# Performance work log

Measured on AMD Instinct MI355X. Metric: run time of the kernel, lower is better.

The kernel has to match this reference:

```python
import jax, jax.numpy as jnp
import numpy as np

N, E, H, D = 50000, 200000, 4, 64  # nodes, directed input edges, heads, hidden_dim
NODE_IN, EDGE_IN = 6, 4


def _ln(x, g, b):
    m = x.mean(-1, keepdims=True)
    v = ((x - m) ** 2).mean(-1, keepdims=True)
    return (x - m) / jnp.sqrt(v + 1e-5) * g + b


def setup_inputs() -> dict:
    key = jax.random.key(0)
    ks = iter(jax.random.split(key, 48))
    def w(i, o):
        return jax.random.normal(next(ks), (i, o), jnp.float32) / np.sqrt(i)
    def b(o):
        return jnp.zeros((o,), jnp.float32)
    return {
        "x": jax.random.normal(next(ks), (N, NODE_IN), jnp.float32),
        "edge_attr": jax.random.normal(next(ks), (E, EDGE_IN), jnp.float32),
        "ne_w1": w(NODE_IN, D), "ne_b1": b(D), "ne_w2": w(D, D), "ne_b2": b(D),
        "ee_w1": w(EDGE_IN, D), "ee_b1": b(D), "ee_w2": w(D, D), "ee_b2": b(D),
        "lnc_g": jnp.ones((2 * D,), jnp.float32), "lnc_b": jnp.zeros((2 * D,), jnp.float32),
        "tq_w": w(2 * D, H * D), "tq_b": b(H * D),
        "tk_w": w(2 * D, H * D), "tk_b": b(H * D),
        "tv_w": w(2 * D, H * D), "tv_b": b(H * D),
        "ts_w": w(2 * D, H * D), "ts_b": b(H * D),
        "lnt_g": jnp.ones((H * D,), jnp.float32), "lnt_b": jnp.zeros((H * D,), jnp.float32),
        "pn_w": w(H * D, D), "pn_b": b(D),
        "pe_w": w(H * D, D), "pe_b": b(D),
        "ec_w1": w(2 * D, D), "ec_b1": b(D), "ec_w2": w(D, 1), "ec_b2": b(1),
        "edge_index": jax.random.randint(next(ks), (2, E), 0, N),
    }


def _forward(x, edge_index, edge_attr, ne_w1, ne_b1, ne_w2, ne_b2,
             ee_w1, ee_b1, ee_w2, ee_b2, lnc_g, lnc_b,
             tq_w, tq_b, tk_w, tk_b, tv_w, tv_b, ts_w, ts_b,
             lnt_g, lnt_b, pn_w, pn_b, pe_w, pe_b,
             ec_w1, ec_b1, ec_w2, ec_b2):
    # bidirectionalize edges
    send = jnp.concatenate([edge_index[0], edge_index[1]])   # [2E]
    recv = jnp.concatenate([edge_index[1], edge_index[0]])   # [2E]
    ea_bi = jnp.concatenate([edge_attr, edge_attr], axis=0)  # [2E, EDGE_IN]
    # 2-layer ReLU MLP encoders (make_mlp with default ReLU output activation)
    node = jax.nn.relu(jax.nn.relu(x @ ne_w1 + ne_b1) @ ne_w2 + ne_b2)        # [N, D]
    edge = jax.nn.relu(jax.nn.relu(ea_bi @ ee_w1 + ee_b1) @ ee_w2 + ee_b2)    # [2E, D]
    for _ in range(1):  # n_iterations = 1
        x0, e0 = node, edge
        agg = jax.ops.segment_sum(edge, recv, num_segments=N)                  # scatter_add
        comb = _ln(jnp.concatenate([node, agg - node], axis=1), lnc_g, lnc_b)  # [N, 2D]
        # TransformerConv(2D -> D, heads=H, concat=True, root_weight=True)
        q = (comb @ tq_w + tq_b).reshape(N, H, D)
        k = (comb @ tk_w + tk_b).reshape(N, H, D)
        v = (comb @ tv_w + tv_b).reshape(N, H, D)
        q_e = q[recv]; k_e = k[send]; v_e = v[send]                            # [2E, H, D]
        score = (q_e * k_e).sum(-1) / np.sqrt(D)                               # [2E, H]
        m = jax.lax.stop_gradient(jax.ops.segment_max(score, recv, num_segments=N))
        ex = jnp.exp(score - m[recv])
        denom = jax.ops.segment_sum(ex, recv, num_segments=N)
        alpha = ex / (denom[recv] + 1e-16)                                     # per-dst softmax
        attn = jax.ops.segment_sum(alpha[:, :, None] * v_e, recv, num_segments=N).reshape(N, H * D)
        outn = _ln(attn + comb @ ts_w + ts_b, lnt_g, lnt_b)                    # skip (root) + LN
        node = outn @ pn_w + pn_b + x0
        edge = (outn[send] - outn[recv]) @ pe_w + pe_b + e0
    start, end = edge_index[0], edge_index[1]
    clf = jnp.concatenate([node[start], node[end]], axis=1)                    # [E, 2D]
    return (jax.nn.relu(clf @ ec_w1 + ec_b1) @ ec_w2 + ec_b2).squeeze(-1)      # [E]


def reference(x, edge_attr, ne_w1, ne_b1, ne_w2, ne_b2, ee_w1, ee_b1, ee_w2, ee_b2,
              lnc_g, lnc_b, tq_w, tq_b, tk_w, tk_b, tv_w, tv_b, ts_w, ts_b,
              lnt_g, lnt_b, pn_w, pn_b, pe_w, pe_b, ec_w1, ec_b1, ec_w2, ec_b2,
              edge_index):
    return _forward(x, edge_index, edge_attr, ne_w1, ne_b1, ne_w2, ne_b2,
                    ee_w1, ee_b1, ee_w2, ee_b2, lnc_g, lnc_b,
                    tq_w, tq_b, tk_w, tk_b, tv_w, tv_b, ts_w, ts_b,
                    lnt_g, lnt_b, pn_w, pn_b, pe_w, pe_b,
                    ec_w1, ec_b1, ec_w2, ec_b2)
```

## Files before the change

### kernel.cpp

```cpp
#include <hip/hip_runtime.h>
#include <hip/hip_bf16.h>


typedef __attribute__((ext_vector_type(8))) short short8;
typedef __attribute__((ext_vector_type(8))) unsigned short u16x8;
typedef __attribute__((ext_vector_type(4))) float f32x4;

__device__ __forceinline__ float wave_reduce_sum(float p) {
  #pragma unroll
  for (int o = 32; o; o >>= 1) p += __shfl_xor(p, o);
  return p;
}
__device__ __forceinline__ ushort f2b(float x) {
  union { float f; unsigned u; } a; a.f = x;
  unsigned r = a.u + 0x7FFF + ((a.u >> 16) & 1);
  return (ushort)(r >> 16);
}
__device__ __forceinline__ float b2f(ushort u) {
  return __uint_as_float((unsigned)u << 16);
}

__global__ __launch_bounds__(256) void node_encoder(
    const float* __restrict__ x, const float* __restrict__ w1,
    const float* __restrict__ b1, const float* __restrict__ w2,
    const float* __restrict__ b2, ushort* __restrict__ out, int N)
{
  __shared__ float sW2[64 * 64];
  __shared__ float sH[4][64];
  int tid = threadIdx.x;
  for (int i = tid; i < 64 * 64; i += 256) sW2[i] = w2[i];
  int wave = tid >> 6, lane = tid & 63;
  int n = blockIdx.x * 4 + wave;
  int nc = n < N ? n : (N - 1);
  float h = b1[lane];
  #pragma unroll
  for (int i = 0; i < 6; ++i) h += x[nc * 6 + i] * w1[i * 64 + lane];
  h = fmaxf(h, 0.f);
  sH[wave][lane] = h;
  __syncthreads();
  float o = b2[lane];
  #pragma unroll 8
  for (int j = 0; j < 64; ++j) o += sH[wave][j] * sW2[j * 64 + lane];
  o = fmaxf(o, 0.f);
  if (n < N) out[n * 64 + lane] = f2b(o);
}

__global__ __launch_bounds__(256) void prep_weights(
    const float* __restrict__ tq_w, const float* __restrict__ tk_w,
    const float* __restrict__ tv_w, const float* __restrict__ ts_w,
    const float* __restrict__ tq_b, const float* __restrict__ tk_b,
    const float* __restrict__ tv_b, const float* __restrict__ ts_b,
    const float* __restrict__ pn_w, const float* __restrict__ ec_w1,
    const float* __restrict__ ee_w2,
    ushort* __restrict__ wqkvsT, float* __restrict__ bqkvs,
    ushort* __restrict__ pnT, ushort* __restrict__ ec1T,
    ushort* __restrict__ ee2T)
{
  int idx = blockIdx.x * 256 + threadIdx.x;
  if (idx < 131072) {
    int p = idx >> 7, k = idx & 127;
    int g, cc;
    if (p < 256) { g = 0; cc = p; }
    else if (p < 768) {
      int d2 = p - 256; int head = d2 >> 7; int ww = d2 & 127;
      int slot = ww >> 3; int o = ww & 7;
      if (o < 4) { g = 1; cc = head * 64 + slot * 4 + o; }
      else       { g = 2; cc = head * 64 + slot * 4 + o - 4; }
    } else { g = 3; cc = p - 768; }
    const float* w = (g == 0) ? tq_w : (g == 1) ? tk_w : (g == 2) ? tv_w : ts_w;
    float v = w[k * 256 + cc];
    if (g == 0) v *= 0.125f;
    wqkvsT[idx] = f2b(v);
  } else if (idx < 147456) {
    int i = idx - 131072; int c = i >> 8, k = i & 255;
    pnT[i] = f2b(pn_w[k * 64 + c]);
  } else if (idx < 155648) {
    int i = idx - 147456; int c = i >> 7, k = i & 127;
    ec1T[i] = f2b(ec_w1[k * 64 + c]);
  } else if (idx < 159744) {
    int i = idx - 155648; int c = i >> 6, k = i & 63;
    ee2T[i] = f2b(ee_w2[k * 64 + c]);
  } else if (idx < 160768) {
    int p = idx - 159744;
    int g, cc;
    if (p < 256) { g = 0; cc = p; }
    else if (p < 768) {
      int d2 = p - 256; int head = d2 >> 7; int ww = d2 & 127;
      int slot = ww >> 3; int o = ww & 7;
      if (o < 4) { g = 1; cc = head * 64 + slot * 4 + o; }
      else       { g = 2; cc = head * 64 + slot * 4 + o - 4; }
    } else { g = 3; cc = p - 768; }
    const float* b = (g == 0) ? tq_b : (g == 1) ? tk_b : (g == 2) ? tv_b : ts_b;
    float v = b[cc];
    if (g == 0) v *= 0.125f;
    bqkvs[p] = v;
  }
}

__global__ __launch_bounds__(256) void deg_count(
    const int* __restrict__ ei, int* __restrict__ deg, int E)
{
  int e = blockIdx.x * 256 + threadIdx.x;
  if (e >= E) return;
  atomicAdd(&deg[ei[e]], 1);
  atomicAdd(&deg[ei[E + e]], 1);
}

__global__ __launch_bounds__(64) void alloc_ranges(
    const int* __restrict__ deg, int* __restrict__ base,
    int* __restrict__ fillcur, int* __restrict__ cursor, int N)
{
  int lane = threadIdx.x;
  int n = blockIdx.x * 64 + lane;
  int d = (n < N) ? deg[n] : 0;
  int s = d;
  #pragma unroll
  for (int o = 1; o < 64; o <<= 1) {
    int t = __shfl_up(s, o);
    if (lane >= o) s += t;
  }
  int tot = __shfl(s, 63);
  int wb = 0;
  if (lane == 63) wb = atomicAdd(cursor, tot);
  wb = __shfl(wb, 63);
  if (n < N) { base[n] = wb + s - d; fillcur[n] = wb + s - d; }
}

__global__ __launch_bounds__(256) void csr_fill(
    const int* __restrict__ ei, int* __restrict__ fillcur,
    int* __restrict__ csr_send, int2* __restrict__ slot2, int E)
{
  int e = blockIdx.x * 256 + threadIdx.x;
  if (e >= E) return;
  int a = ei[e], b = ei[E + e];
  int pa = atomicAdd(&fillcur[b], 1);
  csr_send[pa] = a;
  int pb = atomicAdd(&fillcur[a], 1);
  csr_send[pb] = b;
  slot2[e] = make_int2(pa, pb);
}

__global__ __launch_bounds__(256) void edge_enc(
    const float* __restrict__ ea, const float* __restrict__ w1,
    const float* __restrict__ b1, const ushort* __restrict__ ee2T,
    const float* __restrict__ b2, const int2* __restrict__ slot2,
    ushort* __restrict__ f_csr, int E)
{
  __shared__ ushort As[64 * 72];
  __shared__ ushort Bs[64 * 72];
  __shared__ ushort fT[64 * 72];
  __shared__ int2 sSlot[64];
  int tid = threadIdx.x;
  int wv = tid >> 6, lane = tid & 63, r16 = lane & 15, g4 = lane >> 4;
  int e0 = blockIdx.x * 64;
  if (tid < 64) {
    int e = e0 + tid;
    if (e < E) sSlot[tid] = slot2[e];
  }
  #pragma unroll
  for (int it = 0; it < 2; ++it) {
    int idx = tid + it * 256;
    int r = idx >> 3, c = idx & 7;
    *(short8*)&Bs[r * 72 + c * 8] = *(const short8*)&ee2T[r * 64 + c * 8];
  }
  {
    int c = tid & 63;
    float w0 = w1[c], w1v = w1[64 + c], w2v = w1[128 + c], w3v = w1[192 + c];
    float bb = b1[c];
    int rbase = tid >> 6;
    #pragma unroll
    for (int i = 0; i < 16; ++i) {
      int r = rbase + i * 4;
      int e = e0 + r; if (e >= E) e = E - 1;
      float4 a = *(const float4*)(ea + (size_t)e * 4);
      float hv = bb + a.x * w0 + a.y * w1v + a.z * w2v + a.w * w3v;
      As[r * 72 + c] = f2b(fmaxf(hv, 0.f));
    }
  }
  __syncthreads();
  f32x4 acc[4] = {};
  #pragma unroll
  for (int kk = 0; kk < 2; ++kk) {
    short8 a = *(const short8*)&As[(wv * 16 + r16) * 72 + kk * 32 + g4 * 8];
    #pragma unroll
    for (int sc = 0; sc < 4; ++sc) {
      short8 b = *(const short8*)&Bs[(sc * 16 + r16) * 72 + kk * 32 + g4 * 8];
      acc[sc] = __builtin_amdgcn_mfma_f32_16x16x32_bf16(a, b, acc[sc], 0, 0, 0);
    }
  }
  #pragma unroll
  for (int sc = 0; sc < 4; ++sc) {
    int c = sc * 16 + r16;
    float bs = b2[c];
    #pragma unroll
    for (int j = 0; j < 4; ++j) {
      int r = wv * 16 + g4 * 4 + j;
      fT[r * 72 + c] = f2b(fmaxf(acc[sc][j] + bs, 0.f));
    }
  }
  __syncthreads();
  int gsub = lane >> 4, l16 = lane & 15;
  #pragma unroll
  for (int rr = 0; rr < 8; ++rr) {
    int r = wv * 16 + rr * 2 + (gsub >> 1);
    int e = e0 + r;
    if (e < E) {
      int slot = (gsub & 1) ? sSlot[r].y : sSlot[r].x;
      *(ushort4*)&f_csr[(size_t)slot * 64 + l16 * 4] =
          *(const ushort4*)&fT[r * 72 + l16 * 4];
    }
  }
}

__global__ __launch_bounds__(256) void comb_gather_ln(
    const ushort* __restrict__ node, const ushort* __restrict__ f_csr,
    const int* __restrict__ base, const int* __restrict__ deg,
    const float* __restrict__ g, const float* __restrict__ b,
    ushort* __restrict__ comb, int N)
{
  int tid = blockIdx.x * 256 + threadIdx.x;
  int n = tid >> 6, lane = tid & 63;
  if (n >= N) return;
  float v0 = b2f(node[(size_t)n * 64 + lane]);
  float a = 0.f;
  int b0 = base[n], dn = deg[n];
  for (int j = 0; j < dn; j += 4) {
    int i1 = b0 + (j + 1 < dn ? j + 1 : j);
    int i2 = b0 + (j + 2 < dn ? j + 2 : j);
    int i3 = b0 + (j + 3 < dn ? j + 3 : j);
    float f0 = b2f(f_csr[(size_t)(b0 + j) * 64 + lane]);
    float f1 = b2f(f_csr[(size_t)i1 * 64 + lane]);
    float f2 = b2f(f_csr[(size_t)i2 * 64 + lane]);
    float f3 = b2f(f_csr[(size_t)i3 * 64 + lane]);
    a += f0;
    if (j + 1 < dn) a += f1;
    if (j + 2 < dn) a += f2;
    if (j + 3 < dn) a += f3;
  }
  float v1 = a - v0;
  float s = wave_reduce_sum(v0 + v1);
  float ss = wave_reduce_sum(v0 * v0 + v1 * v1);
  float mean = s * (1.f / 128.f);
  float var = ss * (1.f / 128.f) - mean * mean;
  float rstd = rsqrtf(var + 1e-5f);
  comb[(size_t)n * 128 + lane]      = f2b((v0 - mean) * rstd * g[lane] + b[lane]);
  comb[(size_t)n * 128 + 64 + lane] = f2b((v1 - mean) * rstd * g[64 + lane] + b[64 + lane]);
}

__global__ __launch_bounds__(256) void qkvs_gemm(
    const ushort* __restrict__ comb, const ushort* __restrict__ wqkvsT,
    const float* __restrict__ bias, ushort* __restrict__ qkvs, int N)
{
  __shared__ ushort As[64 * 136];
  __shared__ ushort Bs[64 * 136];
  __shared__ ushort Os[64 * 68];
  int tid = threadIdx.x;
  int wv = tid >> 6, lane = tid & 63, r16 = lane & 15, g4 = lane >> 4;
  int row0 = blockIdx.x * 64;
  #pragma unroll
  for (int it = 0; it < 4; ++it) {
    int idx = tid + it * 256;
    int r = idx >> 4, c = idx & 15;
    int gr = row0 + r; if (gr >= N) gr = N - 1;
    *(short8*)&As[r * 136 + c * 8] = *(const short8*)&comb[(size_t)gr * 128 + c * 8];
    *(short8*)&Bs[r * 136 + c * 8] = *(const short8*)&wqkvsT[(size_t)r * 128 + c * 8];
  }
  __syncthreads();
  for (int ct = 0; ct < 16; ++ct) {
    short8 pf[4];
    if (ct < 15) {
      #pragma unroll
      for (int it = 0; it < 4; ++it) {
        int idx = tid + it * 256;
        int r = idx >> 4, c = idx & 15;
        pf[it] = *(const short8*)&wqkvsT[(size_t)((ct + 1) * 64 + r) * 128 + c * 8];
      }
    }
    f32x4 acc[4] = {};
    #pragma unroll
    for (int kk = 0; kk < 4; ++kk) {
      short8 a = *(const short8*)&As[(wv * 16 + r16) * 136 + kk * 32 + g4 * 8];
      #pragma unroll
      for (int sc = 0; sc < 4; ++sc) {
        short8 b = *(const short8*)&Bs[(sc * 16 + r16) * 136 + kk * 32 + g4 * 8];
        acc[sc] = __builtin_amdgcn_mfma_f32_16x16x32_bf16(a, b, acc[sc], 0, 0, 0);
      }
    }
    __syncthreads();
    if (ct < 15) {
      #pragma unroll
      for (int it = 0; it < 4; ++it) {
        int idx = tid + it * 256;
        int r = idx >> 4, c = idx & 15;
        *(short8*)&Bs[r * 136 + c * 8] = pf[it];
      }
    }
    #pragma unroll
    for (int sc = 0; sc < 4; ++sc) {
      float bs = bias[ct * 64 + sc * 16 + r16];
      #pragma unroll
      for (int j = 0; j < 4; ++j)
        Os[(wv * 16 + g4 * 4 + j) * 68 + sc * 16 + r16] = f2b(acc[sc][j] + bs);
    }
    __syncthreads();
    #pragma unroll
    for (int it = 0; it < 2; ++it) {
      int idx = tid + it * 256;
      int r = idx >> 3, ch = idx & 7;
      int gr = row0 + r;
      if (gr < N)
        *(short8*)&qkvs[(size_t)gr * 1024 + ct * 64 + ch * 8] =
            *(const short8*)&Os[r * 68 + ch * 8];
    }
  }
}

__global__ __launch_bounds__(256) void mgemm(
    const ushort* __restrict__ A, int lda, int M,
    const ushort* __restrict__ BT, const float* __restrict__ bias, int K,
    ushort* __restrict__ outB, int ldo,
    const ushort* __restrict__ res, int ldres, int doRelu)
{
  __shared__ ushort As[64 * 136];
  __shared__ ushort Bs[64 * 136];
  __shared__ ushort Os[64 * 68];
  int tid = threadIdx.x;
  int wv = tid >> 6, lane = tid & 63;
  int r16 = lane & 15, g4 = lane >> 4;
  int row0 = blockIdx.x * 64, col0 = blockIdx.y * 64;
  f32x4 acc[4] = {};
  for (int k0 = 0; k0 < K; k0 += 128) {
    int BK = K - k0; if (BK > 128) BK = 128;
    int csh = (BK == 64) ? 3 : 4;
    int cmask = (1 << csh) - 1;
    int tot = 64 << csh;
    for (int idx = tid; idx < tot; idx += 256) {
      int r = idx >> csh, c = idx & cmask;
      int gr = row0 + r; if (gr >= M) gr = M - 1;
      *(short8*)&As[r * 136 + c * 8] =
          *(const short8*)&A[(size_t)gr * lda + k0 + c * 8];
      *(short8*)&Bs[r * 136 + c * 8] =
          *(const short8*)&BT[(size_t)(col0 + r) * K + k0 + c * 8];
    }
    __syncthreads();
    int ks = BK >> 5;
    for (int kk = 0; kk < ks; ++kk) {
      short8 a = *(const short8*)&As[(wv * 16 + r16) * 136 + kk * 32 + g4 * 8];
      #pragma unroll
      for (int ct = 0; ct < 4; ++ct) {
        short8 b = *(const short8*)&Bs[(ct * 16 + r16) * 136 + kk * 32 + g4 * 8];
        acc[ct] = __builtin_amdgcn_mfma_f32_16x16x32_bf16(a, b, acc[ct], 0, 0, 0);
      }
    }
    __syncthreads();
  }
  #pragma unroll
  for (int ct = 0; ct < 4; ++ct) {
    int c = col0 + ct * 16 + r16;
    float bs = bias[c];
    #pragma unroll
    for (int j = 0; j < 4; ++j) {
      int r = row0 + wv * 16 + g4 * 4 + j;
      int rc = r < M ? r : M - 1;
      float vv = acc[ct][j] + bs;
      if (doRelu) vv = fmaxf(vv, 0.f);
      if (res) vv += b2f(res[(size_t)rc * ldres + c]);
      Os[(wv * 16 + g4 * 4 + j) * 68 + ct * 16 + r16] = f2b(vv);
    }
  }
  __syncthreads();
  #pragma unroll
  for (int it = 0; it < 2; ++it) {
    int idx = tid + it * 256;
    int r = idx >> 3, ch = idx & 7;
    int gr = row0 + r;
    if (gr < M)
      *(short8*)&outB[(size_t)gr * ldo + col0 + ch * 8] =
          *(const short8*)&Os[r * 68 + ch * 8];
  }
}

__global__ __launch_bounds__(256) void attn_ln2(
    ushort* __restrict__ qkvs, const int* __restrict__ base,
    const int* __restrict__ deg, const int* __restrict__ csr_send,
    const float* __restrict__ g, const float* __restrict__ bb, int N)
{
  int tid = blockIdx.x * 256 + threadIdx.x;
  int n = tid >> 6, lane = tid & 63;
  if (n >= N) return;
  int dbase = (lane >> 4) * 64 + (lane & 15) * 4;
  int kvoff = 256 + (lane >> 4) * 128 + (lane & 15) * 8;
  ushort4 qu = *(const ushort4*)(qkvs + (size_t)n * 1024 + dbase);
  float q0 = b2f(qu.x), q1 = b2f(qu.y), q2 = b2f(qu.z), q3 = b2f(qu.w);
  float l = 0.f, a0 = 0.f, a1 = 0.f, a2 = 0.f, a3 = 0.f;
  int b0 = base[n], dn = deg[n];
  for (int j = 0; j < dn; j += 4) {
    int i1 = b0 + (j + 1 < dn ? j + 1 : j);
    int i2 = b0 + (j + 2 < dn ? j + 2 : j);
    int i3 = b0 + (j + 3 < dn ? j + 3 : j);
    int s0 = csr_send[b0 + j], s1 = csr_send[i1];
    int s2 = csr_send[i2], s3 = csr_send[i3];
    u16x8 kv0 = *(const u16x8*)(qkvs + (size_t)s0 * 1024 + kvoff);
    u16x8 kv1 = *(const u16x8*)(qkvs + (size_t)s1 * 1024 + kvoff);
    u16x8 kv2 = *(const u16x8*)(qkvs + (size_t)s2 * 1024 + kvoff);
    u16x8 kv3 = *(const u16x8*)(qkvs + (size_t)s3 * 1024 + kvoff);
    float p0 = q0 * b2f((ushort)kv0[0]) + q1 * b2f((ushort)kv0[1]) +
               q2 * b2f((ushort)kv0[2]) + q3 * b2f((ushort)kv0[3]);
    float p1 = q0 * b2f((ushort)kv1[0]) + q1 * b2f((ushort)kv1[1]) +
               q2 * b2f((ushort)kv1[2]) + q3 * b2f((ushort)kv1[3]);
    float p2 = q0 * b2f((ushort)kv2[0]) + q1 * b2f((ushort)kv2[1]) +
               q2 * b2f((ushort)kv2[2]) + q3 * b2f((ushort)kv2[3]);
    float p3 = q0 * b2f((ushort)kv3[0]) + q1 * b2f((ushort)kv3[1]) +
               q2 * b2f((ushort)kv3[2]) + q3 * b2f((ushort)kv3[3]);
    #pragma unroll
    for (int o = 1; o < 16; o <<= 1) {
      p0 += __shfl_xor(p0, o); p1 += __shfl_xor(p1, o);
      p2 += __shfl_xor(p2, o); p3 += __shfl_xor(p3, o);
    }
    float e0 = __expf(p0);
    float e1 = (j + 1 < dn) ? __expf(p1) : 0.f;
    float e2 = (j + 2 < dn) ? __expf(p2) : 0.f;
    float e3 = (j + 3 < dn) ? __expf(p3) : 0.f;
    l += e0 + e1 + e2 + e3;
    a0 += e0 * b2f((ushort)kv0[4]) + e1 * b2f((ushort)kv1[4]) +
          e2 * b2f((ushort)kv2[4]) + e3 * b2f((ushort)kv3[4]);
    a1 += e0 * b2f((ushort)kv0[5]) + e1 * b2f((ushort)kv1[5]) +
          e2 * b2f((ushort)kv2[5]) + e3 * b2f((ushort)kv3[5]);
    a2 += e0 * b2f((ushort)kv0[6]) + e1 * b2f((ushort)kv1[6]) +
          e2 * b2f((ushort)kv2[6]) + e3 * b2f((ushort)kv3[6]);
    a3 += e0 * b2f((ushort)kv0[7]) + e1 * b2f((ushort)kv1[7]) +
          e2 * b2f((ushort)kv2[7]) + e3 * b2f((ushort)kv3[7]);
  }
  ushort4 su = *(const ushort4*)(qkvs + (size_t)n * 1024 + 768 + dbase);
  float rl = 1.f / (l + 1e-16f);
  float y0 = a0 * rl + b2f(su.x), y1 = a1 * rl + b2f(su.y);
  float y2 = a2 * rl + b2f(su.z), y3 = a3 * rl + b2f(su.w);
  float s1 = wave_reduce_sum(y0 + y1 + y2 + y3);
  float s2 = wave_reduce_sum(y0 * y0 + y1 * y1 + y2 * y2 + y3 * y3);
  float mean = s1 * (1.f / 256.f);
  float var = s2 * (1.f / 256.f) - mean * mean;
  float rstd = rsqrtf(var + 1e-5f);
  ushort4 o;
  o.x = f2b((y0 - mean) * rstd * g[dbase + 0] + bb[dbase + 0]);
  o.y = f2b((y1 - mean) * rstd * g[dbase + 1] + bb[dbase + 1]);
  o.z = f2b((y2 - mean) * rstd * g[dbase + 2] + bb[dbase + 2]);
  o.w = f2b((y3 - mean) * rstd * g[dbase + 3] + bb[dbase + 3]);
  *(ushort4*)(qkvs + (size_t)n * 1024 + dbase) = o;
}

__global__ __launch_bounds__(256) void clf_fused(
    const ushort* __restrict__ nodeB, const int* __restrict__ ei,
    const ushort* __restrict__ ec1T, const float* __restrict__ b1,
    const float* __restrict__ w2, const float* __restrict__ b2v,
    float* __restrict__ out, int E)
{
  __shared__ ushort As[64 * 136];
  __shared__ ushort Bs[64 * 136];
  int tid = threadIdx.x;
  int wv = tid >> 6, lane = tid & 63;
  int r16 = lane & 15, g4 = lane >> 4;
  int e0 = blockIdx.x * 64;
  for (int idx = tid; idx < 1024; idx += 256) {
    int r = idx >> 4, c = idx & 15;
    int e = e0 + r; if (e >= E) e = E - 1;
    int node = (c < 8) ? ei[e] : ei[E + e];
    *(short8*)&As[r * 136 + c * 8] =
        *(const short8*)&nodeB[(size_t)node * 64 + (c & 7) * 8];
    *(short8*)&Bs[r * 136 + c * 8] = *(const short8*)&ec1T[r * 128 + c * 8];
  }
  __syncthreads();
  f32x4 acc[4] = {};
  #pragma unroll
  for (int kk = 0; kk < 4; ++kk) {
    short8 a = *(const short8*)&As[(wv * 16 + r16) * 136 + kk * 32 + g4 * 8];
    #pragma unroll
    for (int ct = 0; ct < 4; ++ct) {
      short8 b = *(const short8*)&Bs[(ct * 16 + r16) * 136 + kk * 32 + g4 * 8];
      acc[ct] = __builtin_amdgcn_mfma_f32_16x16x32_bf16(a, b, acc[ct], 0, 0, 0);
    }
  }
  float p0 = 0.f, p1 = 0.f, p2 = 0.f, p3 = 0.f;
  #pragma unroll
  for (int ct = 0; ct < 4; ++ct) {
    int c = ct * 16 + r16;
    float bb1 = b1[c], ww = w2[c];
    p0 += fmaxf(acc[ct][0] + bb1, 0.f) * ww;
    p1 += fmaxf(acc[ct][1] + bb1, 0.f) * ww;
    p2 += fmaxf(acc[ct][2] + bb1, 0.f) * ww;
    p3 += fmaxf(acc[ct][3] + bb1, 0.f) * ww;
  }
  float part[4] = {p0, p1, p2, p3};
  #pragma unroll
  for (int j = 0; j < 4; ++j) {
    float p = part[j];
    p += __shfl_xor(p, 1); p += __shfl_xor(p, 2);
    p += __shfl_xor(p, 4); p += __shfl_xor(p, 8);
    int r = e0 + wv * 16 + g4 * 4 + j;
    if (r16 == 0 && r < E) out[r] = p + b2v[0];
  }
}

extern "C" void kernel_launch(void* const* d_in, const int* in_sizes, int n_in,
                              void* d_out, int out_size, void* d_ws, size_t ws_size,
                              hipStream_t stream)
{
  const float* x     = (const float*)d_in[0];
  const float* ea    = (const float*)d_in[1];
  const float* ne_w1 = (const float*)d_in[2];
  const float* ne_b1 = (const float*)d_in[3];
  const float* ne_w2 = (const float*)d_in[4];
  const float* ne_b2 = (const float*)d_in[5];
  const float* ee_w1 = (const float*)d_in[6];
  const float* ee_b1 = (const float*)d_in[7];
  const float* ee_w2 = (const float*)d_in[8];
  const float* ee_b2 = (const float*)d_in[9];
  const float* lnc_g = (const float*)d_in[10];
  const float* lnc_b = (const float*)d_in[11];
  const float* tq_w  = (const float*)d_in[12];
  const float* tq_b  = (const float*)d_in[13];
  const float* tk_w  = (const float*)d_in[14];
  const float* tk_b  = (const float*)d_in[15];
  const float* tv_w  = (const float*)d_in[16];
  const float* tv_b  = (const float*)d_in[17];
  const float* ts_w  = (const float*)d_in[18];
  const float* ts_b  = (const float*)d_in[19];
  const float* lnt_g = (const float*)d_in[20];
  const float* lnt_b = (const float*)d_in[21];
  const float* pn_w  = (const float*)d_in[22];
  const float* pn_b  = (const float*)d_in[23];
  const float* ec_w1 = (const float*)d_in[26];
  const float* ec_b1 = (const float*)d_in[27];
  const float* ec_w2 = (const float*)d_in[28];
  const float* ec_b2 = (const float*)d_in[29];
  const int*   ei    = (const int*)d_in[30];

  const int N = in_sizes[0] / 6;
  const int E = in_sizes[1] / 4;
  float* out = (float*)d_out;

  char* w = (char*)d_ws;
  size_t off = 0;
  auto alloc = [&](size_t bytes) -> char* {
    char* p = w + off;
    off = (off + bytes + 255) & ~(size_t)255;
    return p;
  };
  ushort* node0   = (ushort*)alloc((size_t)N * 64 * 2);
  ushort* comb    = (ushort*)alloc((size_t)N * 128 * 2);
  ushort* qkvs    = (ushort*)alloc((size_t)N * 1024 * 2);
  ushort* f_csr   = (ushort*)alloc((size_t)2 * E * 64 * 2);
  ushort* nodeB   = (ushort*)alloc((size_t)N * 64 * 2);
  ushort* wqkvsT  = (ushort*)alloc(1024 * 128 * 2);
  float*  bqkvs   = (float*)alloc(1024 * 4);
  ushort* pnT     = (ushort*)alloc(64 * 256 * 2);
  ushort* ec1T    = (ushort*)alloc(64 * 128 * 2);
  ushort* ee2T    = (ushort*)alloc(64 * 64 * 2);
  int* deg      = (int*)alloc((size_t)N * 4);
  int* base     = (int*)alloc((size_t)N * 4);
  int* fillcur  = (int*)alloc((size_t)N * 4);
  int* csr_send = (int*)alloc((size_t)2 * E * 4);
  int2* slot2   = (int2*)alloc((size_t)E * 8);
  int* cursor   = (int*)alloc(256);

  hipMemsetAsync(deg, 0, (size_t)N * 4, stream);
  hipMemsetAsync(cursor, 0, 4, stream);

  prep_weights<<<(160768 + 255) / 256, 256, 0, stream>>>(
      tq_w, tk_w, tv_w, ts_w, tq_b, tk_b, tv_b, ts_b, pn_w, ec_w1, ee_w2,
      wqkvsT, bqkvs, pnT, ec1T, ee2T);
  node_encoder<<<(N + 3) / 4, 256, 0, stream>>>(x, ne_w1, ne_b1, ne_w2, ne_b2, node0, N);
  deg_count<<<(E + 255) / 256, 256, 0, stream>>>(ei, deg, E);
  alloc_ranges<<<(N + 63) / 64, 64, 0, stream>>>(deg, base, fillcur, cursor, N);
  csr_fill<<<(E + 255) / 256, 256, 0, stream>>>(ei, fillcur, csr_send, slot2, E);
  edge_enc<<<(E + 63) / 64, 256, 0, stream>>>(ea, ee_w1, ee_b1, ee2T, ee_b2,
                                              slot2, f_csr, E);
  comb_gather_ln<<<(N * 64 + 255) / 256, 256, 0, stream>>>(
      node0, f_csr, base, deg, lnc_g, lnc_b, comb, N);
  qkvs_gemm<<<(N + 63) / 64, 256, 0, stream>>>(comb, wqkvsT, bqkvs, qkvs, N);
  attn_ln2<<<(N * 64 + 255) / 256, 256, 0, stream>>>(
      qkvs, base, deg, csr_send, lnt_g, lnt_b, N);
  mgemm<<<dim3((N + 63) / 64, 1), 256, 0, stream>>>(
      qkvs, 1024, N, pnT, pn_b, 256, nodeB, 64, node0, 64, 0);
  clf_fused<<<(E + 63) / 64, 256, 0, stream>>>(
      nodeB, ei, ec1T, ec_b1, ec_w2, ec_b2, out, E);
}
```

Before: 271.4 us.

## Store K/V in FP8 and split Q, KV, skip into separate buffers

The QKVS GEMM now writes K and V as interleaved FP8 bytes into a compact 512-byte-per-node buffer, while Q and skip go to their own bf16 buffers. The attention kernel gathers the smaller FP8 K/V rows per incoming edge and unpacks them with hardware FP8-to-float conversions. This halves the random-gather traffic in the attention step and shrinks the intermediate writes. The cost is lower precision for keys and values, which adds error to the softmax and the aggregation.

```diff
diff --git a/kernel.cpp b/kernel.cpp
--- a/kernel.cpp
+++ b/kernel.cpp
@@ -3,7 +3,7 @@
 
 
 typedef __attribute__((ext_vector_type(8))) short short8;
-typedef __attribute__((ext_vector_type(8))) unsigned short u16x8;
+typedef __attribute__((ext_vector_type(2))) float f32x2;
 typedef __attribute__((ext_vector_type(4))) float f32x4;
 
 __device__ __forceinline__ float wave_reduce_sum(float p) {
@@ -249,7 +249,8 @@
 
 __global__ __launch_bounds__(256) void qkvs_gemm(
     const ushort* __restrict__ comb, const ushort* __restrict__ wqkvsT,
-    const float* __restrict__ bias, ushort* __restrict__ qkvs, int N)
+    const float* __restrict__ bias, ushort* __restrict__ qbuf,
+    unsigned char* __restrict__ kv8, ushort* __restrict__ sbuf, int N)
 {
   __shared__ ushort As[64 * 136];
   __shared__ ushort Bs[64 * 136];
@@ -295,22 +296,48 @@
         *(short8*)&Bs[r * 136 + c * 8] = pf[it];
       }
     }
-    #pragma unroll
-    for (int sc = 0; sc < 4; ++sc) {
-      float bs = bias[ct * 64 + sc * 16 + r16];
+    bool isKV = (ct >= 4 && ct < 12);
+    if (isKV) {
+      unsigned char* Os8 = (unsigned char*)Os;
       #pragma unroll
-      for (int j = 0; j < 4; ++j)
-        Os[(wv * 16 + g4 * 4 + j) * 68 + sc * 16 + r16] = f2b(acc[sc][j] + bs);
+      for (int sc = 0; sc < 4; ++sc) {
+        float bs = bias[ct * 64 + sc * 16 + r16];
+        #pragma unroll
+        for (int j = 0; j < 4; ++j) {
+          float vv = acc[sc][j] + bs;
+          int pk = __builtin_amdgcn_cvt_pk_fp8_f32(vv, vv, 0, false);
+          Os8[(wv * 16 + g4 * 4 + j) * 80 + sc * 16 + r16] = (unsigned char)pk;
+        }
+      }
+    } else {
+      #pragma unroll
+      for (int sc = 0; sc < 4; ++sc) {
+        float bs = bias[ct * 64 + sc * 16 + r16];
+        #pragma unroll
+        for (int j = 0; j < 4; ++j)
+          Os[(wv * 16 + g4 * 4 + j) * 68 + sc * 16 + r16] = f2b(acc[sc][j] + bs);
+      }
     }
     __syncthreads();
-    #pragma unroll
-    for (int it = 0; it < 2; ++it) {
-      int idx = tid + it * 256;
-      int r = idx >> 3, ch = idx & 7;
+    if (isKV) {
+      const unsigned char* Os8 = (const unsigned char*)Os;
+      int r = tid >> 2, ch = tid & 3;
       int gr = row0 + r;
       if (gr < N)
-        *(short8*)&qkvs[(size_t)gr * 1024 + ct * 64 + ch * 8] =
-            *(const short8*)&Os[r * 68 + ch * 8];
+        *(short8*)&kv8[(size_t)gr * 512 + (ct - 4) * 64 + ch * 16] =
+            *(const short8*)&Os8[r * 80 + ch * 16];
+    } else {
+      ushort* dst = (ct < 4) ? qbuf : sbuf;
+      int cb = (ct < 4) ? ct : ct - 12;
+      #pragma unroll
+      for (int it = 0; it < 2; ++it) {
+        int idx = tid + it * 256;
+        int r = idx >> 3, ch = idx & 7;
+        int gr = row0 + r;
+        if (gr < N)
+          *(short8*)&dst[(size_t)gr * 256 + cb * 64 + ch * 8] =
+              *(const short8*)&Os[r * 68 + ch * 8];
+      }
     }
   }
 }
@@ -381,7 +408,8 @@
 }
 
 __global__ __launch_bounds__(256) void attn_ln2(
-    ushort* __restrict__ qkvs, const int* __restrict__ base,
+    ushort* __restrict__ qbuf, const unsigned char* __restrict__ kv8,
+    const ushort* __restrict__ sbuf, const int* __restrict__ base,
     const int* __restrict__ deg, const int* __restrict__ csr_send,
     const float* __restrict__ g, const float* __restrict__ bb, int N)
 {
@@ -389,8 +417,8 @@
   int n = tid >> 6, lane = tid & 63;
   if (n >= N) return;
   int dbase = (lane >> 4) * 64 + (lane & 15) * 4;
-  int kvoff = 256 + (lane >> 4) * 128 + (lane & 15) * 8;
-  ushort4 qu = *(const ushort4*)(qkvs + (size_t)n * 1024 + dbase);
+  int kvoff = (lane >> 4) * 128 + (lane & 15) * 8;
+  ushort4 qu = *(const ushort4*)(qbuf + (size_t)n * 256 + dbase);
   float q0 = b2f(qu.x), q1 = b2f(qu.y), q2 = b2f(qu.z), q3 = b2f(qu.w);
   float l = 0.f, a0 = 0.f, a1 = 0.f, a2 = 0.f, a3 = 0.f;
   int b0 = base[n], dn = deg[n];
@@ -400,18 +428,22 @@
     int i3 = b0 + (j + 3 < dn ? j + 3 : j);
     int s0 = csr_send[b0 + j], s1 = csr_send[i1];
     int s2 = csr_send[i2], s3 = csr_send[i3];
-    u16x8 kv0 = *(const u16x8*)(qkvs + (size_t)s0 * 1024 + kvoff);
-    u16x8 kv1 = *(const u16x8*)(qkvs + (size_t)s1 * 1024 + kvoff);
-    u16x8 kv2 = *(const u16x8*)(qkvs + (size_t)s2 * 1024 + kvoff);
-    u16x8 kv3 = *(const u16x8*)(qkvs + (size_t)s3 * 1024 + kvoff);
-    float p0 = q0 * b2f((ushort)kv0[0]) + q1 * b2f((ushort)kv0[1]) +
-               q2 * b2f((ushort)kv0[2]) + q3 * b2f((ushort)kv0[3]);
-    float p1 = q0 * b2f((ushort)kv1[0]) + q1 * b2f((ushort)kv1[1]) +
-               q2 * b2f((ushort)kv1[2]) + q3 * b2f((ushort)kv1[3]);
-    float p2 = q0 * b2f((ushort)kv2[0]) + q1 * b2f((ushort)kv2[1]) +
-               q2 * b2f((ushort)kv2[2]) + q3 * b2f((ushort)kv2[3]);
-    float p3 = q0 * b2f((ushort)kv3[0]) + q1 * b2f((ushort)kv3[1]) +
-               q2 * b2f((ushort)kv3[2]) + q3 * b2f((ushort)kv3[3]);
+    uint2 kv0 = *(const uint2*)(kv8 + (size_t)s0 * 512 + kvoff);
+    uint2 kv1 = *(const uint2*)(kv8 + (size_t)s1 * 512 + kvoff);
+    uint2 kv2 = *(const uint2*)(kv8 + (size_t)s2 * 512 + kvoff);
+    uint2 kv3 = *(const uint2*)(kv8 + (size_t)s3 * 512 + kvoff);
+    f32x2 kA0 = __builtin_amdgcn_cvt_pk_f32_fp8(kv0.x, false);
+    f32x2 kA1 = __builtin_amdgcn_cvt_pk_f32_fp8(kv0.x, true);
+    f32x2 kB0 = __builtin_amdgcn_cvt_pk_f32_fp8(kv1.x, false);
+    f32x2 kB1 = __builtin_amdgcn_cvt_pk_f32_fp8(kv1.x, true);
+    f32x2 kC0 = __builtin_amdgcn_cvt_pk_f32_fp8(kv2.x, false);
+    f32x2 kC1 = __builtin_amdgcn_cvt_pk_f32_fp8(kv2.x, true);
+    f32x2 kD0 = __builtin_amdgcn_cvt_pk_f32_fp8(kv3.x, false);
+    f32x2 kD1 = __builtin_amdgcn_cvt_pk_f32_fp8(kv3.x, true);
+    float p0 = q0 * kA0[0] + q1 * kA0[1] + q2 * kA1[0] + q3 * kA1[1];
+    float p1 = q0 * kB0[0] + q1 * kB0[1] + q2 * kB1[0] + q3 * kB1[1];
+    float p2 = q0 * kC0[0] + q1 * kC0[1] + q2 * kC1[0] + q3 * kC1[1];
+    float p3 = q0 * kD0[0] + q1 * kD0[1] + q2 * kD1[0] + q3 * kD1[1];
     #pragma unroll
     for (int o = 1; o < 16; o <<= 1) {
       p0 += __shfl_xor(p0, o); p1 += __shfl_xor(p1, o);
@@ -422,16 +454,20 @@
     float e2 = (j + 2 < dn) ? __expf(p2) : 0.f;
     float e3 = (j + 3 < dn) ? __expf(p3) : 0.f;
     l += e0 + e1 + e2 + e3;
-    a0 += e0 * b2f((ushort)kv0[4]) + e1 * b2f((ushort)kv1[4]) +
-          e2 * b2f((ushort)kv2[4]) + e3 * b2f((ushort)kv3[4]);
-    a1 += e0 * b2f((ushort)kv0[5]) + e1 * b2f((ushort)kv1[5]) +
-          e2 * b2f((ushort)kv2[5]) + e3 * b2f((ushort)kv3[5]);
-    a2 += e0 * b2f((ushort)kv0[6]) + e1 * b2f((ushort)kv1[6]) +
-          e2 * b2f((ushort)kv2[6]) + e3 * b2f((ushort)kv3[6]);
-    a3 += e0 * b2f((ushort)kv0[7]) + e1 * b2f((ushort)kv1[7]) +
-          e2 * b2f((ushort)kv2[7]) + e3 * b2f((ushort)kv3[7]);
-  }
-  ushort4 su = *(const ushort4*)(qkvs + (size_t)n * 1024 + 768 + dbase);
+    f32x2 vA0 = __builtin_amdgcn_cvt_pk_f32_fp8(kv0.y, false);
+    f32x2 vA1 = __builtin_amdgcn_cvt_pk_f32_fp8(kv0.y, true);
+    f32x2 vB0 = __builtin_amdgcn_cvt_pk_f32_fp8(kv1.y, false);
+    f32x2 vB1 = __builtin_amdgcn_cvt_pk_f32_fp8(kv1.y, true);
+    f32x2 vC0 = __builtin_amdgcn_cvt_pk_f32_fp8(kv2.y, false);
+    f32x2 vC1 = __builtin_amdgcn_cvt_pk_f32_fp8(kv2.y, true);
+    f32x2 vD0 = __builtin_amdgcn_cvt_pk_f32_fp8(kv3.y, false);
+    f32x2 vD1 = __builtin_amdgcn_cvt_pk_f32_fp8(kv3.y, true);
+    a0 += e0 * vA0[0] + e1 * vB0[0] + e2 * vC0[0] + e3 * vD0[0];
+    a1 += e0 * vA0[1] + e1 * vB0[1] + e2 * vC0[1] + e3 * vD0[1];
+    a2 += e0 * vA1[0] + e1 * vB1[0] + e2 * vC1[0] + e3 * vD1[0];
+    a3 += e0 * vA1[1] + e1 * vB1[1] + e2 * vC1[1] + e3 * vD1[1];
+  }
+  ushort4 su = *(const ushort4*)(sbuf + (size_t)n * 256 + dbase);
   float rl = 1.f / (l + 1e-16f);
   float y0 = a0 * rl + b2f(su.x), y1 = a1 * rl + b2f(su.y);
   float y2 = a2 * rl + b2f(su.z), y3 = a3 * rl + b2f(su.w);
@@ -445,7 +481,7 @@
   o.y = f2b((y1 - mean) * rstd * g[dbase + 1] + bb[dbase + 1]);
   o.z = f2b((y2 - mean) * rstd * g[dbase + 2] + bb[dbase + 2]);
   o.w = f2b((y3 - mean) * rstd * g[dbase + 3] + bb[dbase + 3]);
-  *(ushort4*)(qkvs + (size_t)n * 1024 + dbase) = o;
+  *(ushort4*)(qbuf + (size_t)n * 256 + dbase) = o;
 }
 
 __global__ __launch_bounds__(256) void clf_fused(
@@ -547,7 +583,9 @@
   };
   ushort* node0   = (ushort*)alloc((size_t)N * 64 * 2);
   ushort* comb    = (ushort*)alloc((size_t)N * 128 * 2);
-  ushort* qkvs    = (ushort*)alloc((size_t)N * 1024 * 2);
+  ushort* qbuf    = (ushort*)alloc((size_t)N * 256 * 2);
+  unsigned char* kv8 = (unsigned char*)alloc((size_t)N * 512);
+  ushort* sbuf    = (ushort*)alloc((size_t)N * 256 * 2);
   ushort* f_csr   = (ushort*)alloc((size_t)2 * E * 64 * 2);
   ushort* nodeB   = (ushort*)alloc((size_t)N * 64 * 2);
   ushort* wqkvsT  = (ushort*)alloc(1024 * 128 * 2);
@@ -576,11 +614,12 @@
                                               slot2, f_csr, E);
   comb_gather_ln<<<(N * 64 + 255) / 256, 256, 0, stream>>>(
       node0, f_csr, base, deg, lnc_g, lnc_b, comb, N);
-  qkvs_gemm<<<(N + 63) / 64, 256, 0, stream>>>(comb, wqkvsT, bqkvs, qkvs, N);
+  qkvs_gemm<<<(N + 63) / 64, 256, 0, stream>>>(
+      comb, wqkvsT, bqkvs, qbuf, kv8, sbuf, N);
   attn_ln2<<<(N * 64 + 255) / 256, 256, 0, stream>>>(
-      qkvs, base, deg, csr_send, lnt_g, lnt_b, N);
+      qbuf, kv8, sbuf, base, deg, csr_send, lnt_g, lnt_b, N);
   mgemm<<<dim3((N + 63) / 64, 1), 256, 0, stream>>>(
-      qkvs, 1024, N, pnT, pn_b, 256, nodeB, 64, node0, 64, 0);
+      qbuf, 256, N, pnT, pn_b, 256, nodeB, 64, node0, 64, 0);
   clf_fused<<<(E + 63) / 64, 256, 0, stream>>>(
       nodeB, ei, ec1T, ec_b1, ec_w2, ec_b2, out, E);
 }
```

New measurement: 250.1 us. -7.9%, faster.
